# Kernel optimization log

Measured on AMD Instinct MI355X. Metric: run time of the kernel, lower is better.

## Reference

```python
import jax, jax.numpy as jnp
import numpy as np

NUM_HEADS = 16
HEAD_DIM = 64
ROPE_BASE = 10000.0


def apply_rope(x):
    # x: [b, s, n_h, h_d]; pairwise rotation as in torchtune RotaryPositionalEmbeddings
    b, s, nh, hd = x.shape
    inv_freq = 1.0 / (ROPE_BASE ** (jnp.arange(0, hd, 2, dtype=jnp.float32) / hd))  # [hd/2]
    angles = jnp.arange(s, dtype=jnp.float32)[:, None] * inv_freq[None, :]          # [s, hd/2]
    cos = jnp.cos(angles)[None, :, None, :]  # [1, s, 1, hd/2]
    sin = jnp.sin(angles)[None, :, None, :]
    xp = x.reshape(b, s, nh, hd // 2, 2)
    x1, x2 = xp[..., 0], xp[..., 1]
    rot = jnp.stack([x1 * cos - x2 * sin, x1 * sin + x2 * cos], axis=-1)
    return rot.reshape(b, s, nh, hd)


def setup_inputs() -> dict:
    key = jax.random.key(0)
    k1, k2 = jax.random.split(key)
    B, S, D = 64, 200, 1024
    x = jax.random.normal(k1, (B, S, D), dtype=jnp.float32)
    # causal mask, realistic for a decoder; True = attend
    mask = jnp.broadcast_to(jnp.tril(jnp.ones((S, S), dtype=bool)), (B, S, S))
    W_qkv = jax.random.normal(k2, (3 * D, D), dtype=jnp.float32) * (1.0 / np.sqrt(D))
    b_qkv = jnp.zeros((3 * D,), dtype=jnp.float32)
    return {"x": x, "mask": mask, "W_qkv": W_qkv, "b_qkv": b_qkv}


def reference(x, mask, W_qkv, b_qkv):
    B, S, D = x.shape
    H, hd = NUM_HEADS, HEAD_DIM
    qkv = x @ W_qkv.T + b_qkv                      # [B, S, 3D]
    qkv = qkv.reshape(B, S, H, 3 * hd)
    q, k, v = jnp.split(qkv, 3, axis=-1)           # each [B, S, H, hd]
    q = apply_rope(q)
    k = apply_rope(k)
    q = q.transpose(0, 2, 1, 3)                    # [B, H, S, hd]
    k = k.transpose(0, 2, 1, 3)
    v = v.transpose(0, 2, 1, 3)
    logits = jnp.einsum("bhqd,bhkd->bhqk", q, k) / jnp.sqrt(jnp.float32(hd))
    logits = jnp.where(mask[:, None, :, :], logits, -jnp.inf)
    attn = jax.nn.softmax(logits, axis=-1)
    out = jnp.einsum("bhqk,bhkd->bhqd", attn, v)   # [B, H, S, hd]
    return out.transpose(0, 2, 1, 3).reshape(B, S, H * hd)
```

## Files before the change

kernel.cpp:

```cpp
#include <hip/hip_runtime.h>
#include <hip/hip_bf16.h>

#define BB 64
#define SS 200
#define DD 1024
#define HH 16
#define HD 64
#define N3 3072
#define MM (BB*SS)
#define KK DD
#define SP 208

using half8 = __attribute__((ext_vector_type(8))) _Float16;
using f32x4 = __attribute__((ext_vector_type(4))) float;

__device__ __forceinline__ void gload16(const void* g, void* l) {
    __builtin_amdgcn_global_load_lds(
        (const __attribute__((address_space(1))) void*)g,
        (__attribute__((address_space(3))) void*)l, 16, 0, 0);
}

__global__ __launch_bounds__(256) void f32_to_f16_kernel(const float* __restrict__ in,
                                                         _Float16* __restrict__ out, int n8) {
    int i = blockIdx.x * 256 + threadIdx.x;
    int stride = gridDim.x * 256;
    for (; i < n8; i += stride) {
        float4 a = ((const float4*)in)[i * 2];
        float4 b = ((const float4*)in)[i * 2 + 1];
        half8 h;
        h[0] = (_Float16)a.x; h[1] = (_Float16)a.y; h[2] = (_Float16)a.z; h[3] = (_Float16)a.w;
        h[4] = (_Float16)b.x; h[5] = (_Float16)b.y; h[6] = (_Float16)b.z; h[7] = (_Float16)b.w;
        ((half8*)out)[i] = h;
    }
}

__global__ __launch_bounds__(256) void rope_table_kernel(float* __restrict__ rope) {
    int t = blockIdx.x * 256 + threadIdx.x;
    if (t >= SS * 32) return;
    int s = t >> 5, i = t & 31;
    float inv = powf(10000.0f, -(float)(2 * i) / 64.0f);
    float ang = (float)s * inv;
    rope[t * 2 + 0] = cosf(ang);
    rope[t * 2 + 1] = sinf(ang);
}

__global__ __launch_bounds__(256) void qkv_gemm_f16_kernel(
    const _Float16* __restrict__ Xh, const _Float16* __restrict__ Wh,
    const float* __restrict__ bias, const float* __restrict__ rope,
    _Float16* __restrict__ qo, _Float16* __restrict__ ko, _Float16* __restrict__ vt)
{
    __shared__ _Float16 As[128 * 32];
    __shared__ _Float16 Bs[128 * 32];

    const int t = threadIdx.x;
    const int w = t >> 6, lane = t & 63;
    const int wm = w >> 1, wn = w & 1;
    const int m0 = blockIdx.y * 128, n0 = blockIdx.x * 128;

    f32x4 acc[4][4];
    #pragma unroll
    for (int i = 0; i < 4; ++i)
        #pragma unroll
        for (int j = 0; j < 4; ++j) acc[i][j] = (f32x4)0.f;

    int srow[2], scol[2], sdst[2];
    #pragma unroll
    for (int c = 0; c < 2; ++c) {
        int slot = c * 256 + t;
        int r = slot >> 2, sl = slot & 3;
        srow[c] = r;
        scol[c] = (sl ^ ((r >> 1) & 3)) << 3;
        sdst[c] = (c * 256 + w * 64) * 8;
    }
    const int arow = wm * 64 + (lane & 15);
    const int brow = wn * 64 + (lane & 15);
    const int kq = lane >> 4;

    for (int kt = 0; kt < KK; kt += 32) {
        __syncthreads();
        #pragma unroll
        for (int c = 0; c < 2; ++c) {
            gload16(Xh + (size_t)(m0 + srow[c]) * KK + kt + scol[c], &As[sdst[c]]);
            gload16(Wh + (size_t)(n0 + srow[c]) * KK + kt + scol[c], &Bs[sdst[c]]);
        }
        __syncthreads();

        half8 af[4], bf[4];
        #pragma unroll
        for (int mi = 0; mi < 4; ++mi) {
            int r = arow + mi * 16;
            af[mi] = *(const half8*)&As[r * 32 + ((kq ^ ((r >> 1) & 3)) << 3)];
        }
        #pragma unroll
        for (int ni = 0; ni < 4; ++ni) {
            int r = brow + ni * 16;
            bf[ni] = *(const half8*)&Bs[r * 32 + ((kq ^ ((r >> 1) & 3)) << 3)];
        }
        #pragma unroll
        for (int mi = 0; mi < 4; ++mi)
            #pragma unroll
            for (int ni = 0; ni < 4; ++ni)
                acc[mi][ni] = __builtin_amdgcn_mfma_f32_16x16x32_f16(af[mi], bf[ni], acc[mi][ni], 0, 0, 0);
    }

    #pragma unroll
    for (int ni = 0; ni < 4; ++ni) {
        int n = n0 + wn * 64 + ni * 16 + (lane & 15);
        float bv = bias[n];
        int h = n / 192;
        int rr = n - h * 192;
        int which = rr >> 6;
        int j = rr & 63;
        int jp = j >> 1;
        #pragma unroll
        for (int mi = 0; mi < 4; ++mi) {
            #pragma unroll
            for (int reg = 0; reg < 4; ++reg) {
                int m = m0 + wm * 64 + mi * 16 + (lane >> 4) * 4 + reg;
                int b_ = m / SS, s_ = m - b_ * SS;
                float v = acc[mi][ni][reg] + bv;
                float p = __shfl_xor(v, 1);
                size_t bh = (size_t)b_ * HH + h;
                if (which == 2) {
                    vt[(bh * HD + j) * SP + s_] = (_Float16)v;
                } else {
                    float2 cs = *(const float2*)&rope[(s_ * 32 + jp) * 2];
                    float o = (j & 1) ? fmaf(p, cs.y, v * cs.x) : fmaf(v, cs.x, -p * cs.y);
                    if (which == 0)
                        qo[(bh * SS + s_) * HD + j] = (_Float16)(o * 0.125f);
                    else
                        ko[(bh * SS + s_) * HD + j] = (_Float16)o;
                }
            }
        }
    }
}

__global__ __launch_bounds__(256) void attn_mfma_kernel(
    const _Float16* __restrict__ q, const _Float16* __restrict__ k,
    const _Float16* __restrict__ vt, float* __restrict__ out)
{
    __shared__ _Float16 Klds[SP * 64];
    __shared__ _Float16 VTlds[64 * SP];
    __shared__ _Float16 Plds[4][32 * 32];

    const int bh = blockIdx.x;
    const int b_ = bh >> 4, h = bh & 15;
    const int t = threadIdx.x;
    const int w = t >> 6, lane = t & 63;
    const int l15 = lane & 15, l4 = lane >> 4;

    const _Float16* kbase = k + (size_t)bh * SS * HD;
    const _Float16* vtbase = vt + (size_t)bh * HD * SP;
    const _Float16* qbase = q + (size_t)bh * SS * HD;

    for (int c = t; c < SP * 8; c += 256) {
        int row = c >> 3, g = c & 7;
        int rowc = row < SS ? row : (SS - 1);
        float4 val = *(const float4*)(kbase + rowc * HD + g * 8);
        *(float4*)&Klds[row * 64 + ((g ^ (row & 7)) * 8)] = val;
    }
    for (int c = t; c < 64 * 26; c += 256) {
        int row = c / 26, g = c - row * 26;
        *(float4*)&VTlds[row * SP + g * 8] = *(const float4*)(vtbase + row * SP + g * 8);
    }
    __syncthreads();

    const int qts[2] = { w, 6 - w };
    const int nqt = (w == 3) ? 1 : 2;

    for (int qi = 0; qi < nqt; ++qi) {
        const int qt = qts[qi];
        const int q0 = qt * 32;

        half8 qf[2][2];
        #pragma unroll
        for (int mt = 0; mt < 2; ++mt)
            #pragma unroll
            for (int ks = 0; ks < 2; ++ks)
                qf[mt][ks] = *(const half8*)(qbase + (size_t)(q0 + mt * 16 + l15) * HD + ks * 32 + l4 * 8);

        float mrow[2][4], lrow[2][4];
        f32x4 oacc[2][4];
        #pragma unroll
        for (int mt = 0; mt < 2; ++mt) {
            #pragma unroll
            for (int r = 0; r < 4; ++r) { mrow[mt][r] = -1e30f; lrow[mt][r] = 0.f; }
            #pragma unroll
            for (int nt = 0; nt < 4; ++nt) oacc[mt][nt] = (f32x4)0.f;
        }

        for (int kt = 0; kt <= qt; ++kt) {
            const int k0 = kt * 32;
            half8 kf[2][2];
            #pragma unroll
            for (int nt = 0; nt < 2; ++nt)
                #pragma unroll
                for (int ks = 0; ks < 2; ++ks) {
                    int row = k0 + nt * 16 + l15;
                    int g = l4 + ks * 4;
                    kf[nt][ks] = *(const half8*)&Klds[row * 64 + ((g ^ (row & 7)) * 8)];
                }
            f32x4 s[2][2];
            #pragma unroll
            for (int mt = 0; mt < 2; ++mt)
                #pragma unroll
                for (int nt = 0; nt < 2; ++nt) {
                    f32x4 a = (f32x4)0.f;
                    a = __builtin_amdgcn_mfma_f32_16x16x32_f16(qf[mt][0], kf[nt][0], a, 0, 0, 0);
                    a = __builtin_amdgcn_mfma_f32_16x16x32_f16(qf[mt][1], kf[nt][1], a, 0, 0, 0);
                    s[mt][nt] = a;
                }
            if (kt == qt) {
                #pragma unroll
                for (int mt = 0; mt < 2; ++mt)
                    #pragma unroll
                    for (int nt = 0; nt < 2; ++nt)
                        #pragma unroll
                        for (int r = 0; r < 4; ++r) {
                            int qq = q0 + mt * 16 + l4 * 4 + r;
                            int kk2 = k0 + nt * 16 + l15;
                            if (kk2 > qq || kk2 >= SS) s[mt][nt][r] = -1e30f;
                        }
            }
            #pragma unroll
            for (int mt = 0; mt < 2; ++mt) {
                #pragma unroll
                for (int r = 0; r < 4; ++r) {
                    float tm = fmaxf(s[mt][0][r], s[mt][1][r]);
                    #pragma unroll
                    for (int off = 8; off > 0; off >>= 1)
                        tm = fmaxf(tm, __shfl_xor(tm, off));
                    float mo = mrow[mt][r];
                    float mn = fmaxf(mo, tm);
                    float sc = __expf(mo - mn);
                    float p0 = __expf(s[mt][0][r] - mn);
                    float p1 = __expf(s[mt][1][r] - mn);
                    s[mt][0][r] = p0; s[mt][1][r] = p1;
                    float rs = p0 + p1;
                    #pragma unroll
                    for (int off = 8; off > 0; off >>= 1)
                        rs += __shfl_xor(rs, off);
                    mrow[mt][r] = mn;
                    lrow[mt][r] = lrow[mt][r] * sc + rs;
                    #pragma unroll
                    for (int nt = 0; nt < 4; ++nt)
                        oacc[mt][nt][r] *= sc;
                }
            }
            #pragma unroll
            for (int mt = 0; mt < 2; ++mt)
                #pragma unroll
                for (int nt = 0; nt < 2; ++nt)
                    #pragma unroll
                    for (int r = 0; r < 4; ++r)
                        Plds[w][(mt * 16 + l4 * 4 + r) * 32 + nt * 16 + l15] = (_Float16)s[mt][nt][r];
            asm volatile("s_waitcnt lgkmcnt(0)" ::: "memory");
            __builtin_amdgcn_sched_barrier(0);
            half8 pa[2], vb[4];
            #pragma unroll
            for (int mt = 0; mt < 2; ++mt)
                pa[mt] = *(const half8*)&Plds[w][(mt * 16 + l15) * 32 + l4 * 8];
            #pragma unroll
            for (int nt = 0; nt < 4; ++nt)
                vb[nt] = *(const half8*)&VTlds[(nt * 16 + l15) * SP + k0 + l4 * 8];
            #pragma unroll
            for (int mt = 0; mt < 2; ++mt)
                #pragma unroll
                for (int nt = 0; nt < 4; ++nt)
                    oacc[mt][nt] = __builtin_amdgcn_mfma_f32_16x16x32_f16(pa[mt], vb[nt], oacc[mt][nt], 0, 0, 0);
        }
        #pragma unroll
        for (int mt = 0; mt < 2; ++mt) {
            #pragma unroll
            for (int r = 0; r < 4; ++r) {
                int s_ = q0 + mt * 16 + l4 * 4 + r;
                if (s_ < SS) {
                    float rinv = 1.0f / lrow[mt][r];
                    #pragma unroll
                    for (int nt = 0; nt < 4; ++nt)
                        out[((size_t)b_ * SS + s_) * DD + h * HD + nt * 16 + l15] = oacc[mt][nt][r] * rinv;
                }
            }
        }
    }
}

extern "C" void kernel_launch(void* const* d_in, const int* in_sizes, int n_in,
                              void* d_out, int out_size, void* d_ws, size_t ws_size,
                              hipStream_t stream) {
    const float* x    = (const float*)d_in[0];
    const float* W    = (const float*)d_in[2];
    const float* bias = (const float*)d_in[3];
    float* out = (float*)d_out;

    char* ws = (char*)d_ws;
    float*    rope = (float*)ws;
    _Float16* Xh   = (_Float16*)(ws + 65536);
    _Float16* Wh   = (_Float16*)(ws + 65536 + 26214400ull);
    _Float16* Qh   = (_Float16*)(ws + 65536 + 26214400ull + 6291456ull);
    _Float16* Kh   = Qh + (size_t)BB * HH * SS * HD;
    _Float16* VTh  = Kh + (size_t)BB * HH * SS * HD;

    f32_to_f16_kernel<<<2048, 256, 0, stream>>>(x, Xh, MM * KK / 8);
    f32_to_f16_kernel<<<1024, 256, 0, stream>>>(W, Wh, N3 * KK / 8);
    rope_table_kernel<<<(SS * 32 + 255) / 256, 256, 0, stream>>>(rope);
    qkv_gemm_f16_kernel<<<dim3(N3 / 128, MM / 128), dim3(256), 0, stream>>>(Xh, Wh, bias, rope, Qh, Kh, VTh);
    attn_mfma_kernel<<<BB * HH, 256, 0, stream>>>(Qh, Kh, VTh, out);
}
```

Measured before the change: 359.0 us.

## Double-buffer QKV GEMM LDS tiles and widen attention key tiles with lazy rescaling

The QKV GEMM now double-buffers its A/B LDS tiles so global-to-LDS loads overlap MFMA work, and raises wave priority around the MFMA blocks. The attention kernel processes 64-key tiles instead of 32, swizzles the P scratch, and skips the online-softmax rescale when the new max stays within a threshold of the running max. Row sums are now reduced once at the end instead of every tile. These changes target load latency stalls and per-tile softmax overhead, at the cost of more LDS, a padded V layout, and extra masked work on the diagonal tile.

After: 356.0 us. Within noise of the previous version (-0.8%).

```diff
diff --git a/kernel.cpp b/kernel.cpp
--- a/kernel.cpp
+++ b/kernel.cpp
@@ -9,7 +9,7 @@
 #define N3 3072
 #define MM (BB*SS)
 #define KK DD
-#define SP 208
+#define SPV 216
 
 using half8 = __attribute__((ext_vector_type(8))) _Float16;
 using f32x4 = __attribute__((ext_vector_type(4))) float;
@@ -44,13 +44,36 @@
     rope[t * 2 + 1] = sinf(ang);
 }
 
+__device__ __forceinline__ void gemm_step(const _Float16* Asb, const _Float16* Bsb,
+                                          int arow, int brow, int kq,
+                                          f32x4 (&acc)[4][4]) {
+    half8 af[4], bf[4];
+    #pragma unroll
+    for (int mi = 0; mi < 4; ++mi) {
+        int r = arow + mi * 16;
+        af[mi] = *(const half8*)&Asb[r * 32 + ((kq ^ ((r >> 1) & 3)) << 3)];
+    }
+    #pragma unroll
+    for (int ni = 0; ni < 4; ++ni) {
+        int r = brow + ni * 16;
+        bf[ni] = *(const half8*)&Bsb[r * 32 + ((kq ^ ((r >> 1) & 3)) << 3)];
+    }
+    __builtin_amdgcn_s_setprio(1);
+    #pragma unroll
+    for (int mi = 0; mi < 4; ++mi)
+        #pragma unroll
+        for (int ni = 0; ni < 4; ++ni)
+            acc[mi][ni] = __builtin_amdgcn_mfma_f32_16x16x32_f16(af[mi], bf[ni], acc[mi][ni], 0, 0, 0);
+    __builtin_amdgcn_s_setprio(0);
+}
+
 __global__ __launch_bounds__(256) void qkv_gemm_f16_kernel(
     const _Float16* __restrict__ Xh, const _Float16* __restrict__ Wh,
     const float* __restrict__ bias, const float* __restrict__ rope,
     _Float16* __restrict__ qo, _Float16* __restrict__ ko, _Float16* __restrict__ vt)
 {
-    __shared__ _Float16 As[128 * 32];
-    __shared__ _Float16 Bs[128 * 32];
+    __shared__ _Float16 As[2][128 * 32];
+    __shared__ _Float16 Bs[2][128 * 32];
 
     const int t = threadIdx.x;
     const int w = t >> 6, lane = t & 63;
@@ -76,31 +99,36 @@
     const int brow = wn * 64 + (lane & 15);
     const int kq = lane >> 4;
 
-    for (int kt = 0; kt < KK; kt += 32) {
-        __syncthreads();
+    const _Float16* Xb = Xh + (size_t)m0 * KK;
+    const _Float16* Wb = Wh + (size_t)n0 * KK;
+
+    #pragma unroll
+    for (int c = 0; c < 2; ++c) {
+        gload16(Xb + (size_t)srow[c] * KK + scol[c], &As[0][sdst[c]]);
+        gload16(Wb + (size_t)srow[c] * KK + scol[c], &Bs[0][sdst[c]]);
+    }
+    asm volatile("s_waitcnt vmcnt(0)" ::: "memory");
+    __builtin_amdgcn_s_barrier();
+
+    for (int kt = 0; kt < KK; kt += 64) {
         #pragma unroll
         for (int c = 0; c < 2; ++c) {
-            gload16(Xh + (size_t)(m0 + srow[c]) * KK + kt + scol[c], &As[sdst[c]]);
-            gload16(Wh + (size_t)(n0 + srow[c]) * KK + kt + scol[c], &Bs[sdst[c]]);
-        }
-        __syncthreads();
-
-        half8 af[4], bf[4];
-        #pragma unroll
-        for (int mi = 0; mi < 4; ++mi) {
-            int r = arow + mi * 16;
-            af[mi] = *(const half8*)&As[r * 32 + ((kq ^ ((r >> 1) & 3)) << 3)];
-        }
-        #pragma unroll
-        for (int ni = 0; ni < 4; ++ni) {
-            int r = brow + ni * 16;
-            bf[ni] = *(const half8*)&Bs[r * 32 + ((kq ^ ((r >> 1) & 3)) << 3)];
-        }
-        #pragma unroll
-        for (int mi = 0; mi < 4; ++mi)
-            #pragma unroll
-            for (int ni = 0; ni < 4; ++ni)
-                acc[mi][ni] = __builtin_amdgcn_mfma_f32_16x16x32_f16(af[mi], bf[ni], acc[mi][ni], 0, 0, 0);
+            gload16(Xb + (size_t)srow[c] * KK + kt + 32 + scol[c], &As[1][sdst[c]]);
+            gload16(Wb + (size_t)srow[c] * KK + kt + 32 + scol[c], &Bs[1][sdst[c]]);
+        }
+        gemm_step(As[0], Bs[0], arow, brow, kq, acc);
+        asm volatile("s_waitcnt vmcnt(0)" ::: "memory");
+        __builtin_amdgcn_s_barrier();
+        if (kt + 64 < KK) {
+            #pragma unroll
+            for (int c = 0; c < 2; ++c) {
+                gload16(Xb + (size_t)srow[c] * KK + kt + 64 + scol[c], &As[0][sdst[c]]);
+                gload16(Wb + (size_t)srow[c] * KK + kt + 64 + scol[c], &Bs[0][sdst[c]]);
+            }
+        }
+        gemm_step(As[1], Bs[1], arow, brow, kq, acc);
+        asm volatile("s_waitcnt vmcnt(0)" ::: "memory");
+        __builtin_amdgcn_s_barrier();
     }
 
     #pragma unroll
@@ -122,7 +150,7 @@
                 float p = __shfl_xor(v, 1);
                 size_t bh = (size_t)b_ * HH + h;
                 if (which == 2) {
-                    vt[(bh * HD + j) * SP + s_] = (_Float16)v;
+                    vt[(bh * HD + j) * SPV + s_] = (_Float16)v;
                 } else {
                     float2 cs = *(const float2*)&rope[(s_ * 32 + jp) * 2];
                     float o = (j & 1) ? fmaf(p, cs.y, v * cs.x) : fmaf(v, cs.x, -p * cs.y);
@@ -140,9 +168,9 @@
     const _Float16* __restrict__ q, const _Float16* __restrict__ k,
     const _Float16* __restrict__ vt, float* __restrict__ out)
 {
-    __shared__ _Float16 Klds[SP * 64];
-    __shared__ _Float16 VTlds[64 * SP];
-    __shared__ _Float16 Plds[4][32 * 32];
+    __shared__ _Float16 Klds[256 * 64];
+    __shared__ _Float16 VTlds[64 * SPV];
+    __shared__ _Float16 Plds[4][32 * 64];
 
     const int bh = blockIdx.x;
     const int b_ = bh >> 4, h = bh & 15;
@@ -151,27 +179,28 @@
     const int l15 = lane & 15, l4 = lane >> 4;
 
     const _Float16* kbase = k + (size_t)bh * SS * HD;
-    const _Float16* vtbase = vt + (size_t)bh * HD * SP;
+    const _Float16* vtbase = vt + (size_t)bh * HD * SPV;
     const _Float16* qbase = q + (size_t)bh * SS * HD;
 
-    for (int c = t; c < SP * 8; c += 256) {
+    for (int c = t; c < 256 * 8; c += 256) {
         int row = c >> 3, g = c & 7;
         int rowc = row < SS ? row : (SS - 1);
         float4 val = *(const float4*)(kbase + rowc * HD + g * 8);
         *(float4*)&Klds[row * 64 + ((g ^ (row & 7)) * 8)] = val;
     }
-    for (int c = t; c < 64 * 26; c += 256) {
-        int row = c / 26, g = c - row * 26;
-        *(float4*)&VTlds[row * SP + g * 8] = *(const float4*)(vtbase + row * SP + g * 8);
+    for (int c = t; c < 64 * 27; c += 256) {
+        int row = c / 27, g = c - row * 27;
+        *(float4*)&VTlds[row * SPV + g * 8] = *(const float4*)(vtbase + row * SPV + g * 8);
     }
     __syncthreads();
 
-    const int qts[2] = { w, 6 - w };
+    const int qts[2] = { (w == 3) ? 6 : w, 5 - w };
     const int nqt = (w == 3) ? 1 : 2;
 
     for (int qi = 0; qi < nqt; ++qi) {
         const int qt = qts[qi];
         const int q0 = qt * 32;
+        const int nkt = (q0 + 95) >> 6;
 
         half8 qf[2][2];
         #pragma unroll
@@ -180,42 +209,47 @@
             for (int ks = 0; ks < 2; ++ks)
                 qf[mt][ks] = *(const half8*)(qbase + (size_t)(q0 + mt * 16 + l15) * HD + ks * 32 + l4 * 8);
 
-        float mrow[2][4], lrow[2][4];
+        float mrow[2][4], lsum[2][4];
         f32x4 oacc[2][4];
         #pragma unroll
         for (int mt = 0; mt < 2; ++mt) {
             #pragma unroll
-            for (int r = 0; r < 4; ++r) { mrow[mt][r] = -1e30f; lrow[mt][r] = 0.f; }
+            for (int r = 0; r < 4; ++r) { mrow[mt][r] = -1e30f; lsum[mt][r] = 0.f; }
             #pragma unroll
             for (int nt = 0; nt < 4; ++nt) oacc[mt][nt] = (f32x4)0.f;
         }
 
-        for (int kt = 0; kt <= qt; ++kt) {
-            const int k0 = kt * 32;
-            half8 kf[2][2];
-            #pragma unroll
-            for (int nt = 0; nt < 2; ++nt)
+        for (int ki = 0; ki < nkt; ++ki) {
+            const int k0 = ki * 64;
+            const bool lastk = (ki == nkt - 1);
+
+            half8 kf[4][2];
+            #pragma unroll
+            for (int nt = 0; nt < 4; ++nt)
                 #pragma unroll
                 for (int ks = 0; ks < 2; ++ks) {
                     int row = k0 + nt * 16 + l15;
                     int g = l4 + ks * 4;
                     kf[nt][ks] = *(const half8*)&Klds[row * 64 + ((g ^ (row & 7)) * 8)];
                 }
-            f32x4 s[2][2];
+            f32x4 s[2][4];
+            __builtin_amdgcn_s_setprio(1);
             #pragma unroll
             for (int mt = 0; mt < 2; ++mt)
                 #pragma unroll
-                for (int nt = 0; nt < 2; ++nt) {
+                for (int nt = 0; nt < 4; ++nt) {
                     f32x4 a = (f32x4)0.f;
                     a = __builtin_amdgcn_mfma_f32_16x16x32_f16(qf[mt][0], kf[nt][0], a, 0, 0, 0);
                     a = __builtin_amdgcn_mfma_f32_16x16x32_f16(qf[mt][1], kf[nt][1], a, 0, 0, 0);
                     s[mt][nt] = a;
                 }
-            if (kt == qt) {
+            __builtin_amdgcn_s_setprio(0);
+
+            if (lastk) {
                 #pragma unroll
                 for (int mt = 0; mt < 2; ++mt)
                     #pragma unroll
-                    for (int nt = 0; nt < 2; ++nt)
+                    for (int nt = 0; nt < 4; ++nt)
                         #pragma unroll
                         for (int r = 0; r < 4; ++r) {
                             int qq = q0 + mt * 16 + l4 * 4 + r;
@@ -223,60 +257,106 @@
                             if (kk2 > qq || kk2 >= SS) s[mt][nt][r] = -1e30f;
                         }
             }
+
             #pragma unroll
             for (int mt = 0; mt < 2; ++mt) {
+                float tmax[4];
+                int ok = 1;
                 #pragma unroll
                 for (int r = 0; r < 4; ++r) {
-                    float tm = fmaxf(s[mt][0][r], s[mt][1][r]);
+                    float tm = fmaxf(fmaxf(s[mt][0][r], s[mt][1][r]),
+                                     fmaxf(s[mt][2][r], s[mt][3][r]));
                     #pragma unroll
                     for (int off = 8; off > 0; off >>= 1)
                         tm = fmaxf(tm, __shfl_xor(tm, off));
-                    float mo = mrow[mt][r];
-                    float mn = fmaxf(mo, tm);
-                    float sc = __expf(mo - mn);
-                    float p0 = __expf(s[mt][0][r] - mn);
-                    float p1 = __expf(s[mt][1][r] - mn);
-                    s[mt][0][r] = p0; s[mt][1][r] = p1;
-                    float rs = p0 + p1;
-                    #pragma unroll
-                    for (int off = 8; off > 0; off >>= 1)
-                        rs += __shfl_xor(rs, off);
-                    mrow[mt][r] = mn;
-                    lrow[mt][r] = lrow[mt][r] * sc + rs;
-                    #pragma unroll
-                    for (int nt = 0; nt < 4; ++nt)
-                        oacc[mt][nt][r] *= sc;
-                }
-            }
+                    tmax[r] = tm;
+                    ok &= (tm <= mrow[mt][r] + 4.0f) ? 1 : 0;
+                }
+                if (__all(ok)) {
+                    #pragma unroll
+                    for (int r = 0; r < 4; ++r) {
+                        float mo = mrow[mt][r];
+                        float ps = 0.f;
+                        #pragma unroll
+                        for (int nt = 0; nt < 4; ++nt) {
+                            float p = __expf(s[mt][nt][r] - mo);
+                            s[mt][nt][r] = p;
+                            ps += p;
+                        }
+                        lsum[mt][r] += ps;
+                    }
+                } else {
+                    #pragma unroll
+                    for (int r = 0; r < 4; ++r) {
+                        float mo = mrow[mt][r];
+                        float mn = fmaxf(mo, tmax[r]);
+                        float sc = __expf(mo - mn);
+                        mrow[mt][r] = mn;
+                        float ps = 0.f;
+                        #pragma unroll
+                        for (int nt = 0; nt < 4; ++nt) {
+                            float p = __expf(s[mt][nt][r] - mn);
+                            s[mt][nt][r] = p;
+                            ps += p;
+                        }
+                        lsum[mt][r] = lsum[mt][r] * sc + ps;
+                        #pragma unroll
+                        for (int nt = 0; nt < 4; ++nt)
+                            oacc[mt][nt][r] *= sc;
+                    }
+                }
+            }
+
             #pragma unroll
             for (int mt = 0; mt < 2; ++mt)
                 #pragma unroll
-                for (int nt = 0; nt < 2; ++nt)
-                    #pragma unroll
-                    for (int r = 0; r < 4; ++r)
-                        Plds[w][(mt * 16 + l4 * 4 + r) * 32 + nt * 16 + l15] = (_Float16)s[mt][nt][r];
-            asm volatile("s_waitcnt lgkmcnt(0)" ::: "memory");
-            __builtin_amdgcn_sched_barrier(0);
-            half8 pa[2], vb[4];
+                for (int nt = 0; nt < 4; ++nt)
+                    #pragma unroll
+                    for (int r = 0; r < 4; ++r) {
+                        int row = mt * 16 + l4 * 4 + r;
+                        int col = nt * 16 + l15;
+                        Plds[w][row * 64 + (((col >> 3) ^ (row & 7)) * 8) + (col & 7)] =
+                            (_Float16)s[mt][nt][r];
+                    }
+
+            half8 pa[2][2], vb[4][2];
             #pragma unroll
             for (int mt = 0; mt < 2; ++mt)
-                pa[mt] = *(const half8*)&Plds[w][(mt * 16 + l15) * 32 + l4 * 8];
+                #pragma unroll
+                for (int ksl = 0; ksl < 2; ++ksl) {
+                    int row = mt * 16 + l15;
+                    pa[mt][ksl] = *(const half8*)&Plds[w][row * 64 + (((ksl * 4 + l4) ^ (row & 7)) * 8)];
+                }
             #pragma unroll
             for (int nt = 0; nt < 4; ++nt)
-                vb[nt] = *(const half8*)&VTlds[(nt * 16 + l15) * SP + k0 + l4 * 8];
+                #pragma unroll
+                for (int ksl = 0; ksl < 2; ++ksl) {
+                    int koff = k0 + ksl * 32 + l4 * 8;
+                    koff = (koff > SPV - 8) ? (SPV - 8) : koff;
+                    vb[nt][ksl] = *(const half8*)&VTlds[(nt * 16 + l15) * SPV + koff];
+                }
+            __builtin_amdgcn_s_setprio(1);
             #pragma unroll
             for (int mt = 0; mt < 2; ++mt)
                 #pragma unroll
-                for (int nt = 0; nt < 4; ++nt)
-                    oacc[mt][nt] = __builtin_amdgcn_mfma_f32_16x16x32_f16(pa[mt], vb[nt], oacc[mt][nt], 0, 0, 0);
-        }
+                for (int nt = 0; nt < 4; ++nt) {
+                    oacc[mt][nt] = __builtin_amdgcn_mfma_f32_16x16x32_f16(pa[mt][0], vb[nt][0], oacc[mt][nt], 0, 0, 0);
+                    oacc[mt][nt] = __builtin_amdgcn_mfma_f32_16x16x32_f16(pa[mt][1], vb[nt][1], oacc[mt][nt], 0, 0, 0);
+                }
+            __builtin_amdgcn_s_setprio(0);
+        }
+
         #pragma unroll
         for (int mt = 0; mt < 2; ++mt) {
             #pragma unroll
             for (int r = 0; r < 4; ++r) {
+                float l = lsum[mt][r];
+                #pragma unroll
+                for (int off = 8; off > 0; off >>= 1)
+                    l += __shfl_xor(l, off);
                 int s_ = q0 + mt * 16 + l4 * 4 + r;
                 if (s_ < SS) {
-                    float rinv = 1.0f / lrow[mt][r];
+                    float rinv = 1.0f / l;
                     #pragma unroll
                     for (int nt = 0; nt < 4; ++nt)
                         out[((size_t)b_ * SS + s_) * DD + h * HD + nt * 16 + l15] = oacc[mt][nt][r] * rinv;
```
